# Optimization experiments

Measured on AMD Instinct MI355X. Metric: run time of the kernel, lower is better.

The kernel has to match this reference:

```python
import jax, jax.numpy as jnp
import numpy as np


def setup_inputs() -> dict:
    key = jax.random.key(0)
    k1, k2 = jax.random.split(key)
    B, S, D, H = 64, 2048, 128, 128
    x = jax.random.normal(k1, (B, S, D), dtype=jnp.float32)
    # net = Linear(D+H -> H) + tanh; torch Linear default init scale ~ 1/sqrt(fan_in)
    W = jax.random.normal(k2, (D + H, H), dtype=jnp.float32) / np.sqrt(D + H)
    b = jnp.zeros((H,), dtype=jnp.float32)
    return {"x": x, "W": W, "b": b}


def reference(x, W, b):
    B, S, D = x.shape
    H = W.shape[1]
    # Split W so we avoid materializing concat(x_t, hidden) each step:
    # net(cat(x_t, h)) = tanh(x_t @ Wx + h @ Wh + b)
    Wx, Wh = W[:D], W[D:]
    # Precompute the input projection for all timesteps in one big GEMM.
    xproj = jnp.einsum("bsd,dh->bsh", x, Wx) + b  # [B, S, H]

    h0 = jnp.zeros((B, H), dtype=x.dtype)

    def step(h, xp_t):
        h_new = jnp.tanh(xp_t + h @ Wh)
        return h_new, h_new

    # scan over time: xproj transposed to [S, B, H]
    hidden, outputs = jax.lax.scan(step, h0, jnp.swapaxes(xproj, 0, 1))
    outputs = jnp.swapaxes(outputs, 0, 1)  # [B, S, H]
    return outputs, hidden
```

## Files before the change

kernel.cpp:

```cpp
#include <hip/hip_runtime.h>

#define BB 64
#define SS 2048
#define DD 128
#define HH 128

typedef float v2f __attribute__((ext_vector_type(2)));

#define PKFMA(acc, a, b) \
    asm("v_pk_fma_f32 %0, %1, %2, %0" : "+v"(acc) : "v"(a), "v"(b))

__device__ __forceinline__ float fast_tanh(float x) {
    float e = __expf(2.0f * x);
    return 1.0f - __fdividef(2.0f, e + 1.0f);
}

__device__ __forceinline__ float quad_allreduce(float v) {
    int a = __builtin_amdgcn_update_dpp(0, __float_as_int(v), 0xB1, 0xF, 0xF, true);
    v += __int_as_float(a);
    int c = __builtin_amdgcn_update_dpp(0, __float_as_int(v), 0x4E, 0xF, 0xF, true);
    v += __int_as_float(c);
    return v;
}

__global__ __launch_bounds__(256, 2)
void xproj_kernel(const float* __restrict__ x, const float* __restrict__ W,
                  const float* __restrict__ bias, float* __restrict__ out) {
    __shared__ __align__(16) float4 wxs[64 * 32];
    __shared__ __align__(16) float4 xsw[128 * 16];
    const int tid = threadIdx.x;
    const int tx  = tid & 15;
    const int ty  = tid >> 4;
    const long row0 = (long)blockIdx.x * 128;

    float acc[8][8];
#pragma unroll
    for (int i = 0; i < 8; ++i)
#pragma unroll
        for (int j = 0; j < 8; ++j) acc[i][j] = 0.f;

    for (int kh = 0; kh < 2; ++kh) {
        {
            const float4* wg = (const float4*)(W + kh * 64 * HH);
#pragma unroll
            for (int i = 0; i < 8; ++i) wxs[tid + i * 256] = wg[tid + i * 256];
        }
        {
#pragma unroll
            for (int i = 0; i < 8; ++i) {
                const int g  = tid + i * 256;
                const int r  = g >> 4;
                const int k4 = g & 15;
                const float4 v = ((const float4*)(x + (row0 + r) * DD + kh * 64))[k4];
                xsw[r * 16 + (k4 ^ ((r >> 3) & 7))] = v;
            }
        }
        __syncthreads();

        for (int k4 = 0; k4 < 16; ++k4) {
            float4 xa[8];
#pragma unroll
            for (int i = 0; i < 8; ++i)
                xa[i] = xsw[(ty * 8 + i) * 16 + (k4 ^ (ty & 7))];
            float4 wa[4][2];
#pragma unroll
            for (int kk = 0; kk < 4; ++kk) {
                wa[kk][0] = wxs[(k4 * 4 + kk) * 32 + tx * 2];
                wa[kk][1] = wxs[(k4 * 4 + kk) * 32 + tx * 2 + 1];
            }
#pragma unroll
            for (int i = 0; i < 8; ++i) {
#pragma unroll
                for (int kk = 0; kk < 4; ++kk) {
                    const float xv = (kk == 0) ? xa[i].x : (kk == 1) ? xa[i].y
                                   : (kk == 2) ? xa[i].z : xa[i].w;
                    acc[i][0] = fmaf(xv, wa[kk][0].x, acc[i][0]);
                    acc[i][1] = fmaf(xv, wa[kk][0].y, acc[i][1]);
                    acc[i][2] = fmaf(xv, wa[kk][0].z, acc[i][2]);
                    acc[i][3] = fmaf(xv, wa[kk][0].w, acc[i][3]);
                    acc[i][4] = fmaf(xv, wa[kk][1].x, acc[i][4]);
                    acc[i][5] = fmaf(xv, wa[kk][1].y, acc[i][5]);
                    acc[i][6] = fmaf(xv, wa[kk][1].z, acc[i][6]);
                    acc[i][7] = fmaf(xv, wa[kk][1].w, acc[i][7]);
                }
            }
        }
        __syncthreads();
    }

    const float4 b0 = ((const float4*)bias)[tx * 2];
    const float4 b1 = ((const float4*)bias)[tx * 2 + 1];
#pragma unroll
    for (int i = 0; i < 8; ++i) {
        const float4 o0 = make_float4(acc[i][0] + b0.x, acc[i][1] + b0.y,
                                      acc[i][2] + b0.z, acc[i][3] + b0.w);
        const float4 o1 = make_float4(acc[i][4] + b1.x, acc[i][5] + b1.y,
                                      acc[i][6] + b1.z, acc[i][7] + b1.w);
        float4* og = (float4*)(out + (row0 + ty * 8 + i) * HH);
        og[tx * 2]     = o0;
        og[tx * 2 + 1] = o1;
    }
}

__global__ __launch_bounds__(256, 1)
void rnn_kernel(const float* __restrict__ W, float* __restrict__ out) {
    const int CH = 16;
    const int NC = SS / CH;

    __shared__ __align__(16) float hos[CH * HH];
    __shared__ __align__(16) float hb[2][HH];

    const int b    = blockIdx.x;
    const int tid  = threadIdx.x;
    const int w    = tid >> 6;
    const int lane = tid & 63;
    const int s    = lane & 3;
    const int jj   = lane >> 2;
    const int j0   = w * 32 + 2 * jj;

    v2f whA[16], whB[16];
#pragma unroll
    for (int m = 0; m < 16; ++m) {
        const int r = m >> 1, u = (m & 1) * 2;
        const int k = 32 * s + (((r + 2 * s) & 7) << 2) + u;
        const float* w0 = W + (long)(DD + k) * HH;
        const float* w1 = W + (long)(DD + k + 1) * HH;
        v2f a; a.x = w0[j0];     a.y = w1[j0];     whA[m] = a;
        v2f bb; bb.x = w0[j0 + 1]; bb.y = w1[j0 + 1]; whB[m] = bb;
    }

    float* const xbase = out + (long)b * SS * HH;

    if (tid < 128) { hb[0][tid] = 0.f; hb[1][tid] = 0.f; }

    v2f xpc[4];
    {
        const float* g = xbase + (4 * s) * HH + j0;
#pragma unroll
        for (int i = 0; i < 4; ++i) xpc[i] = *(const v2f*)(g + i * HH);
    }
    __syncthreads();

    for (int c = 0; c < NC; ++c) {
#pragma unroll
        for (int tt = 0; tt < CH; ++tt) {
            const int t = c * CH + tt;
            const float4* hv = (const float4*)hb[(t + 1) & 1];

            v2f A0 = {0.f, 0.f}, A1 = {0.f, 0.f};
            v2f B0 = {0.f, 0.f}, B1 = {0.f, 0.f};
#pragma unroll
            for (int r = 0; r < 8; ++r) {
                const float4 h4 = hv[8 * s + ((r + 2 * s) & 7)];
                v2f hlo; hlo.x = h4.x; hlo.y = h4.y;
                v2f hhi; hhi.x = h4.z; hhi.y = h4.w;
                PKFMA(A0, hlo, whA[2 * r]);
                PKFMA(A1, hhi, whA[2 * r + 1]);
                PKFMA(B0, hlo, whB[2 * r]);
                PKFMA(B1, hhi, whB[2 * r + 1]);
            }
            const v2f SA = A0 + A1;
            const v2f SB = B0 + B1;
            float fA = SA.x + SA.y;
            float fB = SB.x + SB.y;
            const bool own = (s == (tt >> 2));
            fA += own ? xpc[tt & 3].x : 0.f;
            fB += own ? xpc[tt & 3].y : 0.f;
            fA = quad_allreduce(fA);
            fB = quad_allreduce(fB);

            const float hx = (s < 2) ? fA : fB;
            const float h  = fast_tanh(hx);
            const int col  = j0 + (s >> 1);
            if ((s & 1) == 0) hb[t & 1][col] = h;
            else              hos[tt * HH + col] = h;
            __syncthreads();
        }

        {
            float4* hg = (float4*)(xbase + c * CH * HH);
            const float4* hl = (const float4*)hos;
            hg[tid]       = hl[tid];
            hg[tid + 256] = hl[tid + 256];
        }
        if (c + 1 < NC) {
            const float* g = xbase + (c + 1) * CH * HH + (4 * s) * HH + j0;
#pragma unroll
            for (int i = 0; i < 4; ++i) xpc[i] = *(const v2f*)(g + i * HH);
        }
        __syncthreads();
    }

    if (tid < 128) {
        out[(long)BB * SS * HH + b * HH + tid] = hb[1][tid];
    }
}

extern "C" void kernel_launch(void* const* d_in, const int* in_sizes, int n_in,
                              void* d_out, int out_size, void* d_ws, size_t ws_size,
                              hipStream_t stream) {
    const float* x    = (const float*)d_in[0];
    const float* W    = (const float*)d_in[1];
    const float* bias = (const float*)d_in[2];
    float* out = (float*)d_out;

    xproj_kernel<<<dim3((BB * SS) / 128), dim3(256), 0, stream>>>(x, W, bias, out);
    rnn_kernel<<<dim3(BB), dim3(256), 0, stream>>>(W, out);
}
```

Before: 699.0 us.

## Stream RNN outputs directly to global, prefetch xproj two chunks ahead, lighten barriers

The recurrent kernel no longer stages hidden outputs in a shared-memory chunk buffer. Each step now writes its output straight to global memory, which removes the per-chunk copy and the extra barrier. The xproj values for the next chunk are prefetched one chunk further ahead, and the per-step __syncthreads is replaced by an lgkmcnt wait plus s_barrier, so outstanding global stores and loads are not drained at every step. Weight registers are loaded with inline asm in a row-pair layout, and the packed FMAs use op_sel to broadcast h, which drops the final horizontal add. The catch is that the custom barrier does not wait on vmcnt, so correctness rests on the xproj reads racing ahead safely of in-flight output stores to other rows.

```diff
diff --git a/kernel.cpp b/kernel.cpp
--- a/kernel.cpp
+++ b/kernel.cpp
@@ -7,8 +7,16 @@
 
 typedef float v2f __attribute__((ext_vector_type(2)));
 
-#define PKFMA(acc, a, b) \
-    asm("v_pk_fma_f32 %0, %1, %2, %0" : "+v"(acc) : "v"(a), "v"(b))
+#define PKBLO(acc, hp, w) \
+    asm("v_pk_fma_f32 %0, %1, %2, %0 op_sel_hi:[0,1,1]" \
+        : "+v"(acc) : "v"(hp), "v"(w))
+#define PKBHI(acc, hp, w) \
+    asm("v_pk_fma_f32 %0, %1, %2, %0 op_sel:[1,0,0] op_sel_hi:[1,1,1]" \
+        : "+v"(acc) : "v"(hp), "v"(w))
+
+#define LDW(var, r, u) { \
+    const float* _p = Whp + (long)(32 * s + kr##r * 4 + (u)) * HH + j0; \
+    asm volatile("global_load_dwordx2 %0, %1, off" : "=&v"(var) : "v"(_p)); }
 
 __device__ __forceinline__ float fast_tanh(float x) {
     float e = __expf(2.0f * x);
@@ -21,6 +29,10 @@
     int c = __builtin_amdgcn_update_dpp(0, __float_as_int(v), 0x4E, 0xF, 0xF, true);
     v += __int_as_float(c);
     return v;
+}
+
+__device__ __forceinline__ void wg_sync_lds() {
+    asm volatile("s_waitcnt lgkmcnt(0)\n\ts_barrier" ::: "memory");
 }
 
 __global__ __launch_bounds__(256, 2)
@@ -107,7 +119,6 @@
     const int CH = 16;
     const int NC = SS / CH;
 
-    __shared__ __align__(16) float hos[CH * HH];
     __shared__ __align__(16) float hb[2][HH];
 
     const int b    = blockIdx.x;
@@ -118,28 +129,40 @@
     const int jj   = lane >> 2;
     const int j0   = w * 32 + 2 * jj;
 
-    v2f whA[16], whB[16];
-#pragma unroll
-    for (int m = 0; m < 16; ++m) {
-        const int r = m >> 1, u = (m & 1) * 2;
-        const int k = 32 * s + (((r + 2 * s) & 7) << 2) + u;
-        const float* w0 = W + (long)(DD + k) * HH;
-        const float* w1 = W + (long)(DD + k + 1) * HH;
-        v2f a; a.x = w0[j0];     a.y = w1[j0];     whA[m] = a;
-        v2f bb; bb.x = w0[j0 + 1]; bb.y = w1[j0 + 1]; whB[m] = bb;
-    }
+    const int kr0 = (0 + 2 * s) & 7, kr1 = (1 + 2 * s) & 7;
+    const int kr2 = (2 + 2 * s) & 7, kr3 = (3 + 2 * s) & 7;
+    const int kr4 = (4 + 2 * s) & 7, kr5 = (5 + 2 * s) & 7;
+    const int kr6 = (6 + 2 * s) & 7, kr7 = (7 + 2 * s) & 7;
+
+    const float* Whp = W + (long)DD * HH;
+
+    v2f w00, w01, w02, w03, w10, w11, w12, w13;
+    v2f w20, w21, w22, w23, w30, w31, w32, w33;
+    v2f w40, w41, w42, w43, w50, w51, w52, w53;
+    v2f w60, w61, w62, w63, w70, w71, w72, w73;
+    LDW(w00,0,0) LDW(w01,0,1) LDW(w02,0,2) LDW(w03,0,3)
+    LDW(w10,1,0) LDW(w11,1,1) LDW(w12,1,2) LDW(w13,1,3)
+    LDW(w20,2,0) LDW(w21,2,1) LDW(w22,2,2) LDW(w23,2,3)
+    LDW(w30,3,0) LDW(w31,3,1) LDW(w32,3,2) LDW(w33,3,3)
+    LDW(w40,4,0) LDW(w41,4,1) LDW(w42,4,2) LDW(w43,4,3)
+    LDW(w50,5,0) LDW(w51,5,1) LDW(w52,5,2) LDW(w53,5,3)
+    LDW(w60,6,0) LDW(w61,6,1) LDW(w62,6,2) LDW(w63,6,3)
+    LDW(w70,7,0) LDW(w71,7,1) LDW(w72,7,2) LDW(w73,7,3)
 
     float* const xbase = out + (long)b * SS * HH;
 
     if (tid < 128) { hb[0][tid] = 0.f; hb[1][tid] = 0.f; }
 
-    v2f xpc[4];
+    v2f xpc[4], nxt[4];
     {
-        const float* g = xbase + (4 * s) * HH + j0;
-#pragma unroll
-        for (int i = 0; i < 4; ++i) xpc[i] = *(const v2f*)(g + i * HH);
-    }
-    __syncthreads();
+        const float* g0 = xbase + (4 * s) * HH + j0;
+        const float* g1 = xbase + (CH + 4 * s) * HH + j0;
+#pragma unroll
+        for (int i = 0; i < 4; ++i) { xpc[i] = *(const v2f*)(g0 + i * HH);
+                                      nxt[i] = *(const v2f*)(g1 + i * HH); }
+    }
+    asm volatile("s_waitcnt vmcnt(0)" ::: "memory");
+    wg_sync_lds();
 
     for (int c = 0; c < NC; ++c) {
 #pragma unroll
@@ -147,48 +170,42 @@
             const int t = c * CH + tt;
             const float4* hv = (const float4*)hb[(t + 1) & 1];
 
-            v2f A0 = {0.f, 0.f}, A1 = {0.f, 0.f};
-            v2f B0 = {0.f, 0.f}, B1 = {0.f, 0.f};
-#pragma unroll
-            for (int r = 0; r < 8; ++r) {
-                const float4 h4 = hv[8 * s + ((r + 2 * s) & 7)];
-                v2f hlo; hlo.x = h4.x; hlo.y = h4.y;
-                v2f hhi; hhi.x = h4.z; hhi.y = h4.w;
-                PKFMA(A0, hlo, whA[2 * r]);
-                PKFMA(A1, hhi, whA[2 * r + 1]);
-                PKFMA(B0, hlo, whB[2 * r]);
-                PKFMA(B1, hhi, whB[2 * r + 1]);
-            }
-            const v2f SA = A0 + A1;
-            const v2f SB = B0 + B1;
-            float fA = SA.x + SA.y;
-            float fB = SB.x + SB.y;
+            v2f P0 = {0.f, 0.f}, P1 = {0.f, 0.f};
+            v2f P2 = {0.f, 0.f}, P3 = {0.f, 0.f};
+#define STEP_R(r) { \
+            const float4 h4 = hv[8 * s + kr##r]; \
+            v2f hlo; hlo.x = h4.x; hlo.y = h4.y; \
+            v2f hhi; hhi.x = h4.z; hhi.y = h4.w; \
+            PKBLO(P0, hlo, w##r##0); \
+            PKBHI(P1, hlo, w##r##1); \
+            PKBLO(P2, hhi, w##r##2); \
+            PKBHI(P3, hhi, w##r##3); }
+            STEP_R(0) STEP_R(1) STEP_R(2) STEP_R(3)
+            STEP_R(4) STEP_R(5) STEP_R(6) STEP_R(7)
+#undef STEP_R
+            const v2f P = (P0 + P1) + (P2 + P3);
+            float fA = P.x, fB = P.y;
             const bool own = (s == (tt >> 2));
             fA += own ? xpc[tt & 3].x : 0.f;
             fB += own ? xpc[tt & 3].y : 0.f;
             fA = quad_allreduce(fA);
             fB = quad_allreduce(fB);
 
-            const float hx = (s < 2) ? fA : fB;
-            const float h  = fast_tanh(hx);
-            const int col  = j0 + (s >> 1);
+            const float h = fast_tanh((s < 2) ? fA : fB);
+            const int col = j0 + (s >> 1);
             if ((s & 1) == 0) hb[t & 1][col] = h;
-            else              hos[tt * HH + col] = h;
-            __syncthreads();
-        }
-
-        {
-            float4* hg = (float4*)(xbase + c * CH * HH);
-            const float4* hl = (const float4*)hos;
-            hg[tid]       = hl[tid];
-            hg[tid + 256] = hl[tid + 256];
+            else              xbase[(long)t * HH + col] = h;
+            wg_sync_lds();
         }
         if (c + 1 < NC) {
-            const float* g = xbase + (c + 1) * CH * HH + (4 * s) * HH + j0;
-#pragma unroll
-            for (int i = 0; i < 4; ++i) xpc[i] = *(const v2f*)(g + i * HH);
-        }
-        __syncthreads();
+#pragma unroll
+            for (int i = 0; i < 4; ++i) xpc[i] = nxt[i];
+            if (c + 2 < NC) {
+                const float* g = xbase + ((long)(c + 2) * CH + 4 * s) * HH + j0;
+#pragma unroll
+                for (int i = 0; i < 4; ++i) nxt[i] = *(const v2f*)(g + i * HH);
+            }
+        }
     }
 
     if (tid < 128) {
```

Measured after the change: 733.4 us. 4.9% more time.
